# Kernel tuning notes

Measured on AMD Instinct MI355X. Metric: run time of the kernel, lower is better.

## Reference

```python
import jax, jax.numpy as jnp
import numpy as np

EPS = 1e-5

def _bn(x, g, b):
    # BatchNorm1d in training mode: stats over (batch, length) dims, biased var
    mean = jnp.mean(x, axis=(0, 2), keepdims=True)
    var = jnp.var(x, axis=(0, 2), keepdims=True)
    return (x - mean) * jax.lax.rsqrt(var + EPS) * g[None, :, None] + b[None, :, None]

def _conv1x1(x, w, b):
    # pointwise Conv1d: [B,C,T] x [O,C] -> [B,O,T]
    return jnp.einsum('bct,oc->bot', x, w) + b[None, :, None]

def setup_inputs() -> dict:
    key = jax.random.key(0)
    ks = jax.random.split(key, 4)
    B, C, T = 32, 1024, 2048
    x = jax.random.normal(ks[0], (B, C, T), dtype=jnp.float32)
    w1 = jax.random.normal(ks[1], (256, 1024), dtype=jnp.float32) * (1.0 / np.sqrt(1024))
    w2 = jax.random.normal(ks[2], (64, 256), dtype=jnp.float32) * (1.0 / np.sqrt(256))
    return {
        'x': x,
        'bn1_g': jnp.ones((1024,), jnp.float32), 'bn1_b': jnp.zeros((1024,), jnp.float32),
        'w1': w1, 'b1': jnp.zeros((256,), jnp.float32),
        'bn2_g': jnp.ones((256,), jnp.float32), 'bn2_b': jnp.zeros((256,), jnp.float32),
        'w2': w2, 'b2': jnp.zeros((64,), jnp.float32),
    }

def reference(x, bn1_g, bn1_b, w1, b1, bn2_g, bn2_b, w2, b2):
    # reduction layer: BN -> 1x1 conv -> ReLU (1024 -> 256)
    h = jax.nn.relu(_conv1x1(_bn(x, bn1_g, bn1_b), w1, b1))
    # out layer: BN -> 1x1 conv, no activation (256 -> 64)
    out = _conv1x1(_bn(h, bn2_g, bn2_b), w2, b2)
    o = out.shape[1]
    mu = out[:, : o // 2, :]
    logvar = out[:, o // 2 :, :]
    return (mu, logvar)
```

## Files before the change

### kernel.cpp

```cpp
#include <hip/hip_runtime.h>

#define B_  32
#define C1  1024
#define C2  256
#define T_  2048
#define EPSF 1e-5f
#define CPAD 72

typedef __attribute__((ext_vector_type(8))) short bf16x8;
typedef __attribute__((ext_vector_type(4))) float f32x4;

static __device__ __forceinline__ unsigned short f2bf(float f) {
    union { float f; unsigned u; } v; v.f = f;
    unsigned r = v.u + 0x7fffu + ((v.u >> 16) & 1u);
    return (unsigned short)(r >> 16);
}
static __device__ __forceinline__ float bf2f(unsigned short h) {
    union { unsigned u; float f; } v; v.u = ((unsigned)h) << 16;
    return v.f;
}
static __device__ __forceinline__ void g2l16(const void* g, void* l) {
    __builtin_amdgcn_global_load_lds(
        (const __attribute__((address_space(1))) unsigned int*)g,
        (__attribute__((address_space(3))) unsigned int*)l, 16, 0, 0);
}

__global__ __launch_bounds__(256) void k_prep(const float* __restrict__ x,
        unsigned short* __restrict__ xT, float* __restrict__ psum, float* __restrict__ psq) {
    __shared__ unsigned short tile[64 * CPAD];
    __shared__ float red[256];
    int ct = blockIdx.x, b = blockIdx.y, tid = threadIdx.x;
    int c0 = ct * 64;
    int cl = tid >> 2, t4 = tid & 3;
    const float* xrow = x + (size_t)b * C1 * T_ + (size_t)(c0 + cl) * T_;
    float s = 0.f, sq = 0.f;
    for (int t0 = 0; t0 < T_; t0 += 64) {
        #pragma unroll
        for (int j = 0; j < 4; ++j) {
            int tl = j * 16 + t4 * 4;
            float4 v = *(const float4*)(xrow + t0 + tl);
            s  += v.x + v.y + v.z + v.w;
            sq += v.x * v.x + v.y * v.y + v.z * v.z + v.w * v.w;
            tile[(tl + 0) * CPAD + cl] = f2bf(v.x);
            tile[(tl + 1) * CPAD + cl] = f2bf(v.y);
            tile[(tl + 2) * CPAD + cl] = f2bf(v.z);
            tile[(tl + 3) * CPAD + cl] = f2bf(v.w);
        }
        __syncthreads();
        #pragma unroll
        for (int j = 0; j < 2; ++j) {
            int w = tid + j * 256;
            int tl = w >> 3, cu = w & 7;
            uint4 vv = *(const uint4*)&tile[tl * CPAD + cu * 8];
            *(uint4*)&xT[((size_t)b * T_ + t0 + tl) * C1 + c0 + cu * 8] = vv;
        }
        __syncthreads();
    }
    red[tid] = s; __syncthreads();
    if (tid < 64)
        psum[(size_t)b * C1 + c0 + tid] = red[4*tid] + red[4*tid+1] + red[4*tid+2] + red[4*tid+3];
    __syncthreads();
    red[tid] = sq; __syncthreads();
    if (tid < 64)
        psq[(size_t)b * C1 + c0 + tid]  = red[4*tid] + red[4*tid+1] + red[4*tid+2] + red[4*tid+3];
}

__global__ void k_scales1(const float* __restrict__ psum, const float* __restrict__ psq,
        const float* __restrict__ g, const float* __restrict__ bb,
        float* __restrict__ scale, float* __restrict__ shift) {
    int c = blockIdx.x * 256 + threadIdx.x;
    float s = 0.f, sq = 0.f;
    for (int b = 0; b < B_; ++b) { s += psum[b * C1 + c]; sq += psq[b * C1 + c]; }
    float n = (float)(B_ * T_);
    float mean = s / n;
    float var  = sq / n - mean * mean;
    float sc   = g[c] * rsqrtf(var + EPSF);
    scale[c] = sc;
    shift[c] = bb[c] - mean * sc;
}

__global__ void k_fold1(const float* __restrict__ w1, const float* __restrict__ b1,
                        const float* __restrict__ scale1, const float* __restrict__ shift1,
                        unsigned short* __restrict__ w1e, float* __restrict__ b1e) {
    int o = blockIdx.x, tid = threadIdx.x;
    float4 w = ((const float4*)(w1 + (size_t)o * C1))[tid];
    int c = tid * 4;
    float p = w.x * shift1[c] + w.y * shift1[c + 1] + w.z * shift1[c + 2] + w.w * shift1[c + 3];
    uint2 pk;
    pk.x = (unsigned)f2bf(w.x * scale1[c])     | ((unsigned)f2bf(w.y * scale1[c + 1]) << 16);
    pk.y = (unsigned)f2bf(w.z * scale1[c + 2]) | ((unsigned)f2bf(w.w * scale1[c + 3]) << 16);
    *((uint2*)(w1e + (size_t)o * C1 + c)) = pk;
    __shared__ float rs[256];
    rs[tid] = p; __syncthreads();
    for (int off = 128; off > 0; off >>= 1) {
        if (tid < off) rs[tid] += rs[tid + off];
        __syncthreads();
    }
    if (tid == 0) b1e[o] = b1[o] + rs[0];
}

__global__ __launch_bounds__(256) void k_gemm1(const unsigned short* __restrict__ xT,
        const unsigned short* __restrict__ w1e, const float* __restrict__ b1e,
        unsigned short* __restrict__ hT) {
    __shared__ unsigned short sA[128 * 32];
    __shared__ unsigned short sB[128 * 32];
    int bm = blockIdx.x, bn = blockIdx.y, b = blockIdx.z;
    int tid = threadIdx.x;
    int wave = tid >> 6, lane = tid & 63;
    int wm = wave >> 1, wn = wave & 1;
    int l15 = lane & 15, q = lane >> 4;
    f32x4 acc[4][4] = {};
    const unsigned short* xblk = xT + ((size_t)b * T_ + (size_t)bn * 128) * C1;
    const unsigned short* wblk = w1e + (size_t)(bm * 128) * C1;

    for (int k0 = 0; k0 < C1; k0 += 32) {
        #pragma unroll
        for (int i = 0; i < 2; ++i) {
            int idx = (wave * 2 + i) * 64 + lane;
            int row = idx >> 2, cq = idx & 3;
            g2l16(wblk + (size_t)row * C1 + k0 + cq * 8, &sA[(wave * 2 + i) * 512]);
            g2l16(xblk + (size_t)row * C1 + k0 + cq * 8, &sB[(wave * 2 + i) * 512]);
        }
        __syncthreads();
        bf16x8 af[4], bfr[4];
        #pragma unroll
        for (int mi = 0; mi < 4; ++mi)
            af[mi] = *((const bf16x8*)&sA[(wm * 64 + mi * 16 + l15) * 32 + q * 8]);
        #pragma unroll
        for (int ni = 0; ni < 4; ++ni)
            bfr[ni] = *((const bf16x8*)&sB[(wn * 64 + ni * 16 + l15) * 32 + q * 8]);
        #pragma unroll
        for (int mi = 0; mi < 4; ++mi)
            #pragma unroll
            for (int ni = 0; ni < 4; ++ni)
                acc[mi][ni] = __builtin_amdgcn_mfma_f32_16x16x32_bf16(af[mi], bfr[ni], acc[mi][ni], 0, 0, 0);
        __syncthreads();
    }
    int obase = bm * 128 + wm * 64;
    int tbase = bn * 128 + wn * 64;
    #pragma unroll
    for (int mi = 0; mi < 4; ++mi) {
        float4 bias = *(const float4*)&b1e[obase + mi * 16 + q * 4];
        #pragma unroll
        for (int ni = 0; ni < 4; ++ni) {
            int t = tbase + ni * 16 + l15;
            float v0 = fmaxf(acc[mi][ni][0] + bias.x, 0.f);
            float v1 = fmaxf(acc[mi][ni][1] + bias.y, 0.f);
            float v2 = fmaxf(acc[mi][ni][2] + bias.z, 0.f);
            float v3 = fmaxf(acc[mi][ni][3] + bias.w, 0.f);
            uint2 pk;
            pk.x = (unsigned)f2bf(v0) | ((unsigned)f2bf(v1) << 16);
            pk.y = (unsigned)f2bf(v2) | ((unsigned)f2bf(v3) << 16);
            *(uint2*)&hT[((size_t)b * T_ + t) * C2 + obase + mi * 16 + q * 4] = pk;
        }
    }
}

__global__ __launch_bounds__(256) void k_stats2h(const unsigned short* __restrict__ hT,
        float* __restrict__ p2s, float* __restrict__ p2q) {
    int tid = threadIdx.x;
    size_t r0 = (size_t)blockIdx.x * 128;
    float s = 0.f, sq = 0.f;
    for (int r = 0; r < 128; ++r) {
        float v = bf2f(hT[(r0 + r) * C2 + tid]);
        s += v; sq += v * v;
    }
    p2s[blockIdx.x * C2 + tid] = s;
    p2q[blockIdx.x * C2 + tid] = sq;
}

__global__ void k_scales2(const float* __restrict__ p2s, const float* __restrict__ p2q,
        const float* __restrict__ g, const float* __restrict__ bb,
        float* __restrict__ scale, float* __restrict__ shift) {
    int c = threadIdx.x;
    float s = 0.f, sq = 0.f;
    for (int i = 0; i < 512; ++i) { s += p2s[i * C2 + c]; sq += p2q[i * C2 + c]; }
    float n = (float)(B_ * T_);
    float mean = s / n;
    float var  = sq / n - mean * mean;
    float sc   = g[c] * rsqrtf(var + EPSF);
    scale[c] = sc;
    shift[c] = bb[c] - mean * sc;
}

__global__ void k_fold2(const float* __restrict__ w2, const float* __restrict__ b2,
                        const float* __restrict__ scale2, const float* __restrict__ shift2,
                        unsigned short* __restrict__ w2e, float* __restrict__ b2e) {
    int o = blockIdx.x, tid = threadIdx.x;
    float w = w2[(size_t)o * C2 + tid];
    float p = w * shift2[tid];
    w2e[(size_t)o * C2 + tid] = f2bf(w * scale2[tid]);
    __shared__ float rs[256];
    rs[tid] = p; __syncthreads();
    for (int off = 128; off > 0; off >>= 1) {
        if (tid < off) rs[tid] += rs[tid + off];
        __syncthreads();
    }
    if (tid == 0) b2e[o] = b2[o] + rs[0];
}

__global__ __launch_bounds__(256) void k_gemm2(const unsigned short* __restrict__ hT,
        const unsigned short* __restrict__ w2e, const float* __restrict__ b2e,
        float* __restrict__ out) {
    __shared__ unsigned short sA[64 * 32];
    __shared__ unsigned short sB[128 * 32];
    int bn = blockIdx.x, b = blockIdx.y;
    int tid = threadIdx.x;
    int wave = tid >> 6, lane = tid & 63;
    int l15 = lane & 15, q = lane >> 4;
    f32x4 acc[4][2] = {};
    const unsigned short* hblk = hT + ((size_t)b * T_ + (size_t)bn * 128) * C2;

    for (int k0 = 0; k0 < C2; k0 += 32) {
        {
            int row = tid >> 2, cq = tid & 3;
            *(uint4*)&sA[row * 32 + cq * 8] = *(const uint4*)(w2e + (size_t)row * C2 + k0 + cq * 8);
        }
        #pragma unroll
        for (int i = 0; i < 2; ++i) {
            int task = tid + i * 256;
            int row = task >> 2, cq = task & 3;
            *(uint4*)&sB[row * 32 + cq * 8] = *(const uint4*)(hblk + (size_t)row * C2 + k0 + cq * 8);
        }
        __syncthreads();
        bf16x8 af[4], bfr[2];
        #pragma unroll
        for (int mi = 0; mi < 4; ++mi)
            af[mi] = *((const bf16x8*)&sA[(mi * 16 + l15) * 32 + q * 8]);
        #pragma unroll
        for (int ni = 0; ni < 2; ++ni)
            bfr[ni] = *((const bf16x8*)&sB[(wave * 32 + ni * 16 + l15) * 32 + q * 8]);
        #pragma unroll
        for (int mi = 0; mi < 4; ++mi)
            #pragma unroll
            for (int ni = 0; ni < 2; ++ni)
                acc[mi][ni] = __builtin_amdgcn_mfma_f32_16x16x32_bf16(af[mi], bfr[ni], acc[mi][ni], 0, 0, 0);
        __syncthreads();
    }
    int tbase = bn * 128 + wave * 32;
    #pragma unroll
    for (int mi = 0; mi < 4; ++mi) {
        #pragma unroll
        for (int reg = 0; reg < 4; ++reg) {
            int o = mi * 16 + q * 4 + reg;
            float bias = b2e[o];
            size_t base = (o < 32)
                ? ((size_t)b * 32 * T_ + (size_t)o * T_)
                : (2097152u + (size_t)b * 32 * T_ + (size_t)(o - 32) * T_);
            #pragma unroll
            for (int ni = 0; ni < 2; ++ni) {
                int t = tbase + ni * 16 + l15;
                out[base + t] = acc[mi][ni][reg] + bias;
            }
        }
    }
}

extern "C" void kernel_launch(void* const* d_in, const int* in_sizes, int n_in,
                              void* d_out, int out_size, void* d_ws, size_t ws_size,
                              hipStream_t stream) {
    const float* x   = (const float*)d_in[0];
    const float* g1  = (const float*)d_in[1];
    const float* bb1 = (const float*)d_in[2];
    const float* w1  = (const float*)d_in[3];
    const float* b1  = (const float*)d_in[4];
    const float* g2  = (const float*)d_in[5];
    const float* bb2 = (const float*)d_in[6];
    const float* w2  = (const float*)d_in[7];
    const float* b2  = (const float*)d_in[8];
    float* out = (float*)d_out;

    char* ws = (char*)d_ws;
    float* scale1 = (float*)(ws + 0);
    float* shift1 = (float*)(ws + 4096);
    float* b1e    = (float*)(ws + 8192);
    float* scale2 = (float*)(ws + 12288);
    float* shift2 = (float*)(ws + 16384);
    float* b2e    = (float*)(ws + 20480);
    float* psum   = (float*)(ws + 24576);
    float* psq    = (float*)(ws + 155648);
    float* p2s    = (float*)(ws + 286720);
    float* p2q    = (float*)(ws + 811008);
    unsigned short* w1e = (unsigned short*)(ws + 1335296);
    unsigned short* w2e = (unsigned short*)(ws + 1859584);
    unsigned short* xT  = (unsigned short*)(ws + 1892352);
    unsigned short* hT  = (unsigned short*)(ws + 1892352 + 134217728);

    k_prep   <<<dim3(16, 32), dim3(256), 0, stream>>>(x, xT, psum, psq);
    k_scales1<<<dim3(4),      dim3(256), 0, stream>>>(psum, psq, g1, bb1, scale1, shift1);
    k_fold1  <<<dim3(256),    dim3(256), 0, stream>>>(w1, b1, scale1, shift1, w1e, b1e);
    k_gemm1  <<<dim3(2, 16, 32), dim3(256), 0, stream>>>(xT, w1e, b1e, hT);
    k_stats2h<<<dim3(512),    dim3(256), 0, stream>>>(hT, p2s, p2q);
    k_scales2<<<dim3(1),      dim3(256), 0, stream>>>(p2s, p2q, g2, bb2, scale2, shift2);
    k_fold2  <<<dim3(64),     dim3(256), 0, stream>>>(w2, b2, scale2, shift2, w2e, b2e);
    k_gemm2  <<<dim3(16, 32), dim3(256), 0, stream>>>(hT, w2e, b2e, out);
}
```

Before: 538.1 us.

## Fuse BN stats into GEMM epilogue, widen GEMM1 tile, merge scale kernels

Computes the second BatchNorm's per-channel sum and sum of squares inside the GEMM1 epilogue with wave shuffles. This removes the separate pass that re-read the bf16 hidden tensor. GEMM1 now covers all 256 output channels per block (128x32 accumulators per wave, launch_bounds 256,2), so the xT tile is loaded once instead of twice. The scale kernels are folded into the weight-fold kernels, and GEMM2 switches to direct global-to-LDS loads. Costs: higher register pressure in GEMM1 and redundant per-block stat reduction in the fold kernels, including a 1024-row loop in fold2. The hidden-layer stats now come from fp32 values before bf16 rounding, which differs slightly from the old path.

After: 536.2 us. Within noise of the previous version (-0.4%).

```diff
diff --git a/kernel.cpp b/kernel.cpp
--- a/kernel.cpp
+++ b/kernel.cpp
@@ -14,10 +14,6 @@
     union { float f; unsigned u; } v; v.f = f;
     unsigned r = v.u + 0x7fffu + ((v.u >> 16) & 1u);
     return (unsigned short)(r >> 16);
-}
-static __device__ __forceinline__ float bf2f(unsigned short h) {
-    union { unsigned u; float f; } v; v.u = ((unsigned)h) << 16;
-    return v.f;
 }
 static __device__ __forceinline__ void g2l16(const void* g, void* l) {
     __builtin_amdgcn_global_load_lds(
@@ -65,30 +61,34 @@
         psq[(size_t)b * C1 + c0 + tid]  = red[4*tid] + red[4*tid+1] + red[4*tid+2] + red[4*tid+3];
 }
 
-__global__ void k_scales1(const float* __restrict__ psum, const float* __restrict__ psq,
-        const float* __restrict__ g, const float* __restrict__ bb,
-        float* __restrict__ scale, float* __restrict__ shift) {
-    int c = blockIdx.x * 256 + threadIdx.x;
-    float s = 0.f, sq = 0.f;
-    for (int b = 0; b < B_; ++b) { s += psum[b * C1 + c]; sq += psq[b * C1 + c]; }
-    float n = (float)(B_ * T_);
-    float mean = s / n;
-    float var  = sq / n - mean * mean;
-    float sc   = g[c] * rsqrtf(var + EPSF);
-    scale[c] = sc;
-    shift[c] = bb[c] - mean * sc;
-}
-
-__global__ void k_fold1(const float* __restrict__ w1, const float* __restrict__ b1,
-                        const float* __restrict__ scale1, const float* __restrict__ shift1,
-                        unsigned short* __restrict__ w1e, float* __restrict__ b1e) {
+__global__ __launch_bounds__(256) void k_fold1(const float* __restrict__ w1,
+        const float* __restrict__ b1, const float* __restrict__ g1, const float* __restrict__ bb1,
+        const float* __restrict__ psum, const float* __restrict__ psq,
+        unsigned short* __restrict__ w1e, float* __restrict__ b1e) {
     int o = blockIdx.x, tid = threadIdx.x;
+    int c = tid * 4;
+    float4 s = {0,0,0,0}, sq = {0,0,0,0};
+    for (int b = 0; b < B_; ++b) {
+        float4 a = *(const float4*)(psum + (size_t)b * C1 + c);
+        float4 q = *(const float4*)(psq  + (size_t)b * C1 + c);
+        s.x += a.x; s.y += a.y; s.z += a.z; s.w += a.w;
+        sq.x += q.x; sq.y += q.y; sq.z += q.z; sq.w += q.w;
+    }
+    const float n = (float)(B_ * T_);
+    float4 gg = *(const float4*)(g1 + c);
+    float4 bv = *(const float4*)(bb1 + c);
+    float m0 = s.x / n, m1 = s.y / n, m2 = s.z / n, m3 = s.w / n;
+    float sc0 = gg.x * rsqrtf(sq.x / n - m0 * m0 + EPSF);
+    float sc1 = gg.y * rsqrtf(sq.y / n - m1 * m1 + EPSF);
+    float sc2 = gg.z * rsqrtf(sq.z / n - m2 * m2 + EPSF);
+    float sc3 = gg.w * rsqrtf(sq.w / n - m3 * m3 + EPSF);
+    float sh0 = bv.x - m0 * sc0, sh1 = bv.y - m1 * sc1;
+    float sh2 = bv.z - m2 * sc2, sh3 = bv.w - m3 * sc3;
     float4 w = ((const float4*)(w1 + (size_t)o * C1))[tid];
-    int c = tid * 4;
-    float p = w.x * shift1[c] + w.y * shift1[c + 1] + w.z * shift1[c + 2] + w.w * shift1[c + 3];
+    float p = w.x * sh0 + w.y * sh1 + w.z * sh2 + w.w * sh3;
     uint2 pk;
-    pk.x = (unsigned)f2bf(w.x * scale1[c])     | ((unsigned)f2bf(w.y * scale1[c + 1]) << 16);
-    pk.y = (unsigned)f2bf(w.z * scale1[c + 2]) | ((unsigned)f2bf(w.w * scale1[c + 3]) << 16);
+    pk.x = (unsigned)f2bf(w.x * sc0) | ((unsigned)f2bf(w.y * sc1) << 16);
+    pk.y = (unsigned)f2bf(w.z * sc2) | ((unsigned)f2bf(w.w * sc3) << 16);
     *((uint2*)(w1e + (size_t)o * C1 + c)) = pk;
     __shared__ float rs[256];
     rs[tid] = p; __syncthreads();
@@ -99,48 +99,54 @@
     if (tid == 0) b1e[o] = b1[o] + rs[0];
 }
 
-__global__ __launch_bounds__(256) void k_gemm1(const unsigned short* __restrict__ xT,
+__global__ __launch_bounds__(256, 2) void k_gemm1(const unsigned short* __restrict__ xT,
         const unsigned short* __restrict__ w1e, const float* __restrict__ b1e,
-        unsigned short* __restrict__ hT) {
-    __shared__ unsigned short sA[128 * 32];
+        unsigned short* __restrict__ hT, float* __restrict__ p2s, float* __restrict__ p2q) {
+    __shared__ unsigned short sA[256 * 32];
     __shared__ unsigned short sB[128 * 32];
-    int bm = blockIdx.x, bn = blockIdx.y, b = blockIdx.z;
+    int bn = blockIdx.x, b = blockIdx.y;
     int tid = threadIdx.x;
     int wave = tid >> 6, lane = tid & 63;
     int wm = wave >> 1, wn = wave & 1;
     int l15 = lane & 15, q = lane >> 4;
-    f32x4 acc[4][4] = {};
+    f32x4 acc[8][4] = {};
     const unsigned short* xblk = xT + ((size_t)b * T_ + (size_t)bn * 128) * C1;
-    const unsigned short* wblk = w1e + (size_t)(bm * 128) * C1;
 
     for (int k0 = 0; k0 < C1; k0 += 32) {
+        #pragma unroll
+        for (int i = 0; i < 4; ++i) {
+            int idx = (wave * 4 + i) * 64 + lane;
+            int row = idx >> 2, cq = idx & 3;
+            g2l16(w1e + (size_t)row * C1 + k0 + cq * 8, &sA[(wave * 4 + i) * 512]);
+        }
         #pragma unroll
         for (int i = 0; i < 2; ++i) {
             int idx = (wave * 2 + i) * 64 + lane;
             int row = idx >> 2, cq = idx & 3;
-            g2l16(wblk + (size_t)row * C1 + k0 + cq * 8, &sA[(wave * 2 + i) * 512]);
             g2l16(xblk + (size_t)row * C1 + k0 + cq * 8, &sB[(wave * 2 + i) * 512]);
         }
         __syncthreads();
-        bf16x8 af[4], bfr[4];
-        #pragma unroll
-        for (int mi = 0; mi < 4; ++mi)
-            af[mi] = *((const bf16x8*)&sA[(wm * 64 + mi * 16 + l15) * 32 + q * 8]);
+        bf16x8 bfr[4];
         #pragma unroll
         for (int ni = 0; ni < 4; ++ni)
             bfr[ni] = *((const bf16x8*)&sB[(wn * 64 + ni * 16 + l15) * 32 + q * 8]);
         #pragma unroll
-        for (int mi = 0; mi < 4; ++mi)
+        for (int mi = 0; mi < 8; ++mi) {
+            bf16x8 af = *((const bf16x8*)&sA[(wm * 128 + mi * 16 + l15) * 32 + q * 8]);
             #pragma unroll
             for (int ni = 0; ni < 4; ++ni)
-                acc[mi][ni] = __builtin_amdgcn_mfma_f32_16x16x32_bf16(af[mi], bfr[ni], acc[mi][ni], 0, 0, 0);
-        __syncthreads();
-    }
-    int obase = bm * 128 + wm * 64;
+                acc[mi][ni] = __builtin_amdgcn_mfma_f32_16x16x32_bf16(af, bfr[ni], acc[mi][ni], 0, 0, 0);
+        }
+        __syncthreads();
+    }
+    int obase = wm * 128;
     int tbase = bn * 128 + wn * 64;
+    int prow = (b * 16 + bn) * 2 + wn;
     #pragma unroll
-    for (int mi = 0; mi < 4; ++mi) {
-        float4 bias = *(const float4*)&b1e[obase + mi * 16 + q * 4];
+    for (int mi = 0; mi < 8; ++mi) {
+        int og = obase + mi * 16 + q * 4;
+        float4 bias = *(const float4*)&b1e[og];
+        float s0 = 0, s1 = 0, s2 = 0, s3 = 0, q0 = 0, q1 = 0, q2 = 0, q3 = 0;
         #pragma unroll
         for (int ni = 0; ni < 4; ++ni) {
             int t = tbase + ni * 16 + l15;
@@ -148,48 +154,44 @@
             float v1 = fmaxf(acc[mi][ni][1] + bias.y, 0.f);
             float v2 = fmaxf(acc[mi][ni][2] + bias.z, 0.f);
             float v3 = fmaxf(acc[mi][ni][3] + bias.w, 0.f);
+            s0 += v0; q0 += v0 * v0;  s1 += v1; q1 += v1 * v1;
+            s2 += v2; q2 += v2 * v2;  s3 += v3; q3 += v3 * v3;
             uint2 pk;
             pk.x = (unsigned)f2bf(v0) | ((unsigned)f2bf(v1) << 16);
             pk.y = (unsigned)f2bf(v2) | ((unsigned)f2bf(v3) << 16);
-            *(uint2*)&hT[((size_t)b * T_ + t) * C2 + obase + mi * 16 + q * 4] = pk;
-        }
-    }
-}
-
-__global__ __launch_bounds__(256) void k_stats2h(const unsigned short* __restrict__ hT,
-        float* __restrict__ p2s, float* __restrict__ p2q) {
-    int tid = threadIdx.x;
-    size_t r0 = (size_t)blockIdx.x * 128;
+            *(uint2*)&hT[((size_t)b * T_ + t) * C2 + og] = pk;
+        }
+        #pragma unroll
+        for (int m = 1; m <= 8; m <<= 1) {
+            s0 += __shfl_xor(s0, m); s1 += __shfl_xor(s1, m);
+            s2 += __shfl_xor(s2, m); s3 += __shfl_xor(s3, m);
+            q0 += __shfl_xor(q0, m); q1 += __shfl_xor(q1, m);
+            q2 += __shfl_xor(q2, m); q3 += __shfl_xor(q3, m);
+        }
+        if (l15 == 0) {
+            *(float4*)&p2s[(size_t)prow * C2 + og] = make_float4(s0, s1, s2, s3);
+            *(float4*)&p2q[(size_t)prow * C2 + og] = make_float4(q0, q1, q2, q3);
+        }
+    }
+}
+
+__global__ __launch_bounds__(256) void k_fold2(const float* __restrict__ w2,
+        const float* __restrict__ b2, const float* __restrict__ g2, const float* __restrict__ bb2,
+        const float* __restrict__ p2s, const float* __restrict__ p2q,
+        unsigned short* __restrict__ w2e, float* __restrict__ b2e) {
+    int o = blockIdx.x, tid = threadIdx.x;
     float s = 0.f, sq = 0.f;
-    for (int r = 0; r < 128; ++r) {
-        float v = bf2f(hT[(r0 + r) * C2 + tid]);
-        s += v; sq += v * v;
-    }
-    p2s[blockIdx.x * C2 + tid] = s;
-    p2q[blockIdx.x * C2 + tid] = sq;
-}
-
-__global__ void k_scales2(const float* __restrict__ p2s, const float* __restrict__ p2q,
-        const float* __restrict__ g, const float* __restrict__ bb,
-        float* __restrict__ scale, float* __restrict__ shift) {
-    int c = threadIdx.x;
-    float s = 0.f, sq = 0.f;
-    for (int i = 0; i < 512; ++i) { s += p2s[i * C2 + c]; sq += p2q[i * C2 + c]; }
-    float n = (float)(B_ * T_);
+    for (int r = 0; r < 1024; ++r) {
+        s  += p2s[(size_t)r * C2 + tid];
+        sq += p2q[(size_t)r * C2 + tid];
+    }
+    const float n = (float)(B_ * T_);
     float mean = s / n;
-    float var  = sq / n - mean * mean;
-    float sc   = g[c] * rsqrtf(var + EPSF);
-    scale[c] = sc;
-    shift[c] = bb[c] - mean * sc;
-}
-
-__global__ void k_fold2(const float* __restrict__ w2, const float* __restrict__ b2,
-                        const float* __restrict__ scale2, const float* __restrict__ shift2,
-                        unsigned short* __restrict__ w2e, float* __restrict__ b2e) {
-    int o = blockIdx.x, tid = threadIdx.x;
+    float sc = g2[tid] * rsqrtf(sq / n - mean * mean + EPSF);
+    float sh = bb2[tid] - mean * sc;
     float w = w2[(size_t)o * C2 + tid];
-    float p = w * shift2[tid];
-    w2e[(size_t)o * C2 + tid] = f2bf(w * scale2[tid]);
+    float p = w * sh;
+    w2e[(size_t)o * C2 + tid] = f2bf(w * sc);
     __shared__ float rs[256];
     rs[tid] = p; __syncthreads();
     for (int off = 128; off > 0; off >>= 1) {
@@ -213,14 +215,15 @@
 
     for (int k0 = 0; k0 < C2; k0 += 32) {
         {
-            int row = tid >> 2, cq = tid & 3;
-            *(uint4*)&sA[row * 32 + cq * 8] = *(const uint4*)(w2e + (size_t)row * C2 + k0 + cq * 8);
+            int idx = wave * 64 + lane;
+            int row = idx >> 2, cq = idx & 3;
+            g2l16(w2e + (size_t)row * C2 + k0 + cq * 8, &sA[wave * 512]);
         }
         #pragma unroll
         for (int i = 0; i < 2; ++i) {
-            int task = tid + i * 256;
-            int row = task >> 2, cq = task & 3;
-            *(uint4*)&sB[row * 32 + cq * 8] = *(const uint4*)(hblk + (size_t)row * C2 + k0 + cq * 8);
+            int idx = (wave * 2 + i) * 64 + lane;
+            int row = idx >> 2, cq = idx & 3;
+            g2l16(hblk + (size_t)row * C2 + k0 + cq * 8, &sB[(wave * 2 + i) * 512]);
         }
         __syncthreads();
         bf16x8 af[4], bfr[2];
@@ -271,27 +274,20 @@
     float* out = (float*)d_out;
 
     char* ws = (char*)d_ws;
-    float* scale1 = (float*)(ws + 0);
-    float* shift1 = (float*)(ws + 4096);
-    float* b1e    = (float*)(ws + 8192);
-    float* scale2 = (float*)(ws + 12288);
-    float* shift2 = (float*)(ws + 16384);
-    float* b2e    = (float*)(ws + 20480);
-    float* psum   = (float*)(ws + 24576);
-    float* psq    = (float*)(ws + 155648);
-    float* p2s    = (float*)(ws + 286720);
-    float* p2q    = (float*)(ws + 811008);
-    unsigned short* w1e = (unsigned short*)(ws + 1335296);
-    unsigned short* w2e = (unsigned short*)(ws + 1859584);
-    unsigned short* xT  = (unsigned short*)(ws + 1892352);
-    unsigned short* hT  = (unsigned short*)(ws + 1892352 + 134217728);
-
-    k_prep   <<<dim3(16, 32), dim3(256), 0, stream>>>(x, xT, psum, psq);
-    k_scales1<<<dim3(4),      dim3(256), 0, stream>>>(psum, psq, g1, bb1, scale1, shift1);
-    k_fold1  <<<dim3(256),    dim3(256), 0, stream>>>(w1, b1, scale1, shift1, w1e, b1e);
-    k_gemm1  <<<dim3(2, 16, 32), dim3(256), 0, stream>>>(xT, w1e, b1e, hT);
-    k_stats2h<<<dim3(512),    dim3(256), 0, stream>>>(hT, p2s, p2q);
-    k_scales2<<<dim3(1),      dim3(256), 0, stream>>>(p2s, p2q, g2, bb2, scale2, shift2);
-    k_fold2  <<<dim3(64),     dim3(256), 0, stream>>>(w2, b2, scale2, shift2, w2e, b2e);
-    k_gemm2  <<<dim3(16, 32), dim3(256), 0, stream>>>(hT, w2e, b2e, out);
-}
+    float* b1e  = (float*)(ws + 0);
+    float* b2e  = (float*)(ws + 4096);
+    float* psum = (float*)(ws + 8192);
+    float* psq  = (float*)(ws + 139264);
+    float* p2s  = (float*)(ws + 270336);
+    float* p2q  = (float*)(ws + 1318912);
+    unsigned short* w1e = (unsigned short*)(ws + 2367488);
+    unsigned short* w2e = (unsigned short*)(ws + 2891776);
+    unsigned short* xT  = (unsigned short*)(ws + 2924544);
+    unsigned short* hT  = (unsigned short*)(ws + 2924544 + 134217728);
+
+    k_prep <<<dim3(16, 32), dim3(256), 0, stream>>>(x, xT, psum, psq);
+    k_fold1<<<dim3(256),    dim3(256), 0, stream>>>(w1, b1, g1, bb1, psum, psq, w1e, b1e);
+    k_gemm1<<<dim3(16, 32), dim3(256), 0, stream>>>(xT, w1e, b1e, hT, p2s, p2q);
+    k_fold2<<<dim3(64),     dim3(256), 0, stream>>>(w2, b2, g2, bb2, p2s, p2q, w2e, b2e);
+    k_gemm2<<<dim3(16, 32), dim3(256), 0, stream>>>(hT, w2e, b2e, out);
+}
```
